# Kernel optimization log

Measured on AMD Instinct MI355X. Metric: run time of the kernel, lower is better.

## Reference

```python
import jax, jax.numpy as jnp
import numpy as np

EPS = 1e-5

def layer_norm(x, g, b):
    mu = jnp.mean(x, axis=-1, keepdims=True)
    var = jnp.mean(jnp.square(x - mu), axis=-1, keepdims=True)
    return (x - mu) * jax.lax.rsqrt(var + EPS) * g + b

def setup_inputs() -> dict:
    key = jax.random.key(0)
    ks = jax.random.split(key, 12)
    I, H, N = 512, 512, 65536
    s = 0.02
    return {
        "x": jax.random.normal(ks[0], (I,), dtype=jnp.float32),
        "hiddens": jax.random.normal(ks[1], (N, H), dtype=jnp.float32),
        "Wz": jax.random.normal(ks[2], (H, I + H), dtype=jnp.float32) * s,
        "Wri": jax.random.normal(ks[3], (H, I), dtype=jnp.float32) * s,
        "Wrh": jax.random.normal(ks[4], (H, H), dtype=jnp.float32) * s,
        "Wu": jax.random.normal(ks[5], (H, I + H), dtype=jnp.float32) * s,
        "gz": jnp.ones((H,), jnp.float32), "bz": jnp.zeros((H,), jnp.float32),
        "gr": jnp.ones((H,), jnp.float32), "br": jnp.zeros((H,), jnp.float32),
        "gu": jnp.ones((H,), jnp.float32), "bu": jnp.zeros((H,), jnp.float32),
    }

def reference(x, hiddens, Wz, Wri, Wrh, Wu, gz, bz, gr, br, gu, bu):
    # hiddens: [N, H] stacked child hidden states; x: [I]
    hidden_sum = hiddens.sum(0)  # [H]
    # r gate: per-child linear + LayerNorm + sigmoid -> [N, H]
    r_pre = x @ Wri.T + hiddens @ Wrh.T  # broadcast input term over children
    r = jax.nn.sigmoid(layer_norm(r_pre, gr, br))
    # z gate over (input, sum of child hiddens)
    z = jax.nn.sigmoid(layer_norm(jnp.concatenate([x, hidden_sum]) @ Wz.T, gz, bz))
    # candidate with reset-gated child sum
    u = jnp.tanh(layer_norm(jnp.concatenate([x, (r * hiddens).sum(0)]) @ Wu.T, gu, bu))
    h = z * hidden_sum + (1.0 - z) * u
    return h
```

## Files before the change

### kernel.cpp

```cpp
#include <hip/hip_runtime.h>

#define HDIM 512
#define BM 128

typedef __attribute__((ext_vector_type(8))) short bf16x8;
typedef __attribute__((ext_vector_type(4))) float f32x4;

__device__ __forceinline__ unsigned short f2bf(float f){
  union { float f; unsigned int u; } c; c.f = f;
  unsigned int u = c.u;
  unsigned int r = u + 0x7fffu + ((u >> 16) & 1u);
  return (unsigned short)(r >> 16);
}
__device__ __forceinline__ float bf2f(unsigned short b){
  union { unsigned int u; float f; } c; c.u = ((unsigned int)b) << 16;
  return c.f;
}
__device__ __forceinline__ unsigned int pack_trunc(float a, float b){
  return __builtin_amdgcn_perm(__float_as_uint(b), __float_as_uint(a), 0x07060302u);
}

__global__ __launch_bounds__(256) void prep_k(const float* __restrict__ Wrh,
    unsigned short* __restrict__ wpack, const float* __restrict__ Wri,
    const float* __restrict__ x, float* __restrict__ xwri)
{
  int b = blockIdx.x;
  if (b < 128){
    int t    = b * 256 + threadIdx.x;
    int lane = t & 63;
    int g    = t >> 6;
    int ni   = g & 3;
    int kkk  = (g >> 2) & 15;
    int wc   = g >> 6;
    int row  = wc * 64 + ni * 16 + (lane & 15);
    int k0   = kkk * 32 + (lane >> 4) * 8;
    const float* src = Wrh + (size_t)row * HDIM + k0;
    float4 f0 = *(const float4*)(src);
    float4 f1 = *(const float4*)(src + 4);
    bf16x8 v;
    v[0]=(short)f2bf(f0.x); v[1]=(short)f2bf(f0.y); v[2]=(short)f2bf(f0.z); v[3]=(short)f2bf(f0.w);
    v[4]=(short)f2bf(f1.x); v[5]=(short)f2bf(f1.y); v[6]=(short)f2bf(f1.z); v[7]=(short)f2bf(f1.w);
    *(bf16x8*)(wpack + (size_t)t * 8) = v;
  } else {
    int lane = threadIdx.x & 63, wid = threadIdx.x >> 6;
    int row = (b - 128) * 4 + wid;
    const float* Wr = Wri + (size_t)row * HDIM;
    float a = 0.f;
    #pragma unroll
    for (int k = 0; k < HDIM / 64; k++) a += x[k*64 + lane] * Wr[k*64 + lane];
    #pragma unroll
    for (int m = 1; m < 64; m <<= 1) a += __shfl_xor(a, m, 64);
    if (lane == 0) xwri[row] = a;
  }
}

__global__ __launch_bounds__(1024, 4) void fused_r(
    const float* __restrict__ hiddens,
    const unsigned short* __restrict__ wpack,
    const float* __restrict__ xWri,
    const float* __restrict__ gr, const float* __restrict__ br,
    float* __restrict__ psum_rh, float* __restrict__ psum_h)
{
  __shared__ short As[BM * HDIM];
  __shared__ float redS[8 * 128];
  __shared__ float redQ[8 * 128];
  __shared__ float mu_s[128], rs_s[128];

  const int tid    = threadIdx.x;
  const int lane   = tid & 63;
  const int wid    = tid >> 6;
  const int rowgrp = wid >> 3;
  const int colgrp = wid & 7;
  const int llo    = lane & 15;
  const int lhi    = lane >> 4;
  const int wcol   = colgrp * 64;
  const int rbase  = rowgrp * 64;
  const int r0     = blockIdx.x * BM;

  const int arow = tid >> 3;
  const int ac8  = (tid & 7) * 8;
  const float* aslice = hiddens + (size_t)(r0 + arow) * HDIM + (tid & 7) * 4;
  char* asb = (char*)As + arow * 1024;
  const int sw = (arow & 7) << 4;

  f32x4 acc[4][4];
  #pragma unroll
  for (int i = 0; i < 4; i++)
    #pragma unroll
    for (int j = 0; j < 4; j++)
      #pragma unroll
      for (int k = 0; k < 4; k++) acc[i][j][k] = 0.f;

  float4 pref0 = *(const float4*)(aslice);
  float4 pref1 = *(const float4*)(aslice + 32);
  const bf16x8* wp = (const bf16x8*)wpack + ((size_t)colgrp * 16 * 4) * 64 + lane;
  bf16x8 bfr[4];
  #pragma unroll
  for (int ni = 0; ni < 4; ni++) bfr[ni] = wp[ni * 64];
  {
    uint2 w; w.x = pack_trunc(pref0.x, pref0.y); w.y = pack_trunc(pref0.z, pref0.w);
    *(uint2*)(asb + (ac8 ^ sw)) = w;
  }
  asm volatile("s_waitcnt lgkmcnt(0)" ::: "memory");
  __builtin_amdgcn_s_barrier();

  #pragma unroll 2
  for (int kb = 0; kb < 16; kb++){
    bf16x8 af[4];
    #pragma unroll
    for (int mi = 0; mi < 4; mi++){
      int row = rbase + mi * 16 + llo;
      af[mi] = *(const bf16x8*)((char*)As + row * 1024
                 + ((kb * 64 + lhi * 16) ^ ((row & 7) << 4)));
    }
    if ((kb & 1) == 0){ if (kb + 2 < 16) pref0 = *(const float4*)(aslice + (kb + 2) * 32); }
    else              { if (kb + 2 < 16) pref1 = *(const float4*)(aslice + (kb + 2) * 32); }
    #pragma unroll
    for (int mi = 0; mi < 4; mi++)
      #pragma unroll
      for (int ni = 0; ni < 4; ni++)
        acc[mi][ni] = __builtin_amdgcn_mfma_f32_16x16x32_bf16(af[mi], bfr[ni], acc[mi][ni], 0, 0, 0);
    if (kb + 1 < 16){
      const bf16x8* wpn = wp + (kb + 1) * 4 * 64;
      #pragma unroll
      for (int ni = 0; ni < 4; ni++) bfr[ni] = wpn[ni * 64];
    }
    if (kb + 1 < 16){
      float4 p = ((kb + 1) & 1) ? pref1 : pref0;
      uint2 w; w.x = pack_trunc(p.x, p.y); w.y = pack_trunc(p.z, p.w);
      *(uint2*)(asb + (((kb + 1) * 64 + ac8) ^ sw)) = w;
    }
    asm volatile("s_waitcnt lgkmcnt(0)" ::: "memory");
    __builtin_amdgcn_s_barrier();
  }

  float xw[4], g4[4], b4[4];
  #pragma unroll
  for (int ni = 0; ni < 4; ni++){
    int c = wcol + ni * 16 + llo;
    xw[ni] = xWri[c];
    g4[ni] = gr[c];
    b4[ni] = br[c];
  }
  #pragma unroll
  for (int mi = 0; mi < 4; mi++){
    #pragma unroll
    for (int rr = 0; rr < 4; rr++){
      float sv = 0.f, qv = 0.f;
      #pragma unroll
      for (int ni = 0; ni < 4; ni++){
        float v = acc[mi][ni][rr] + xw[ni];
        acc[mi][ni][rr] = v;
        sv += v; qv += v * v;
      }
      #pragma unroll
      for (int m = 1; m < 16; m <<= 1){
        sv += __shfl_xor(sv, m, 64);
        qv += __shfl_xor(qv, m, 64);
      }
      if (llo == 0){
        int row = rbase + mi * 16 + lhi * 4 + rr;
        redS[colgrp * 128 + row] = sv;
        redQ[colgrp * 128 + row] = qv;
      }
    }
  }
  __syncthreads();
  if (tid < 128){
    float S = 0.f, Q = 0.f;
    #pragma unroll
    for (int w = 0; w < 8; w++){ S += redS[w * 128 + tid]; Q += redQ[w * 128 + tid]; }
    float mu  = S * (1.f / 512.f);
    float var = Q * (1.f / 512.f) - mu * mu;
    mu_s[tid] = mu;
    rs_s[tid] = rsqrtf(var + 1e-5f);
  }
  __syncthreads();

  float prh[4] = {0.f, 0.f, 0.f, 0.f};
  float ph [4] = {0.f, 0.f, 0.f, 0.f};
  #pragma unroll
  for (int mi = 0; mi < 4; mi++){
    #pragma unroll
    for (int rr = 0; rr < 4; rr++){
      int row = rbase + mi * 16 + lhi * 4 + rr;
      float mu = mu_s[row], rs = rs_s[row];
      int sw2 = (row & 7) << 4;
      #pragma unroll
      for (int ni = 0; ni < 4; ni++){
        float v = (acc[mi][ni][rr] - mu) * rs * g4[ni] + b4[ni];
        float r = __builtin_amdgcn_rcpf(1.f + __expf(-v));
        int col = wcol + ni * 16 + llo;
        float h = bf2f(*(const unsigned short*)((char*)As + row * 1024 + ((col * 2) ^ sw2)));
        prh[ni] += r * h;
        ph [ni] += h;
      }
    }
  }
  #pragma unroll
  for (int ni = 0; ni < 4; ni++){
    prh[ni] += __shfl_xor(prh[ni], 16, 64);
    prh[ni] += __shfl_xor(prh[ni], 32, 64);
    ph [ni] += __shfl_xor(ph [ni], 16, 64);
    ph [ni] += __shfl_xor(ph [ni], 32, 64);
  }
  float* ppRH = redS;
  float* ppH  = redQ;
  if (lhi == 0){
    #pragma unroll
    for (int ni = 0; ni < 4; ni++){
      int col = wcol + ni * 16 + llo;
      ppRH[rowgrp * 512 + col] = prh[ni];
      ppH [rowgrp * 512 + col] = ph[ni];
    }
  }
  __syncthreads();
  if (tid < 512){
    psum_rh[(size_t)blockIdx.x * HDIM + tid] = ppRH[tid] + ppRH[512 + tid];
    psum_h [(size_t)blockIdx.x * HDIM + tid] = ppH[tid]  + ppH[512 + tid];
  }
}

__global__ __launch_bounds__(256) void reduce_psums(
    const float* __restrict__ psum_rh, const float* __restrict__ psum_h,
    const float* __restrict__ x, float* __restrict__ catz, float* __restrict__ catu,
    int nblk)
{
  __shared__ float L[8][32];
  int b = blockIdx.x, t = threadIdx.x;
  if (b < 32){
    const float* P = (b < 16) ? psum_rh : psum_h;
    int c0 = (b & 15) * 32;
    int wj = t >> 5, ci = t & 31;
    float a = 0.f;
    for (int s = wj; s < nblk; s += 8) a += P[(size_t)s * 512 + c0 + ci];
    L[wj][ci] = a;
    __syncthreads();
    if (t < 32){
      float r = 0.f;
      #pragma unroll
      for (int w = 0; w < 8; w++) r += L[w][t];
      if (b < 16) catu[512 + c0 + t] = r;
      else        catz[512 + c0 + t] = r;
    }
  } else {
    int i = ((b - 32) & 1) * 256 + t;
    if (b < 34) catz[i] = x[i];
    else        catu[i] = x[i];
  }
}

__global__ __launch_bounds__(256) void matvec_zu(
    const float* __restrict__ Wz, const float* __restrict__ Wu,
    const float* __restrict__ catz, const float* __restrict__ catu,
    float* __restrict__ zpre, float* __restrict__ upre)
{
  int b = blockIdx.x, lane = threadIdx.x & 63, wid = threadIdx.x >> 6;
  int row = (b & 127) * 4 + wid;
  const float* W = (b < 128) ? Wz : Wu;
  const float* v = (b < 128) ? catz : catu;
  float*       o = (b < 128) ? zpre : upre;
  const float* Wr = W + (size_t)row * 1024;
  float a = 0.f;
  #pragma unroll
  for (int k = 0; k < 1024 / 64; k++) a += v[k*64 + lane] * Wr[k*64 + lane];
  #pragma unroll
  for (int m = 1; m < 64; m <<= 1) a += __shfl_xor(a, m, 64);
  if (lane == 0) o[row] = a;
}

__global__ __launch_bounds__(512) void finalize_k(
    const float* __restrict__ zpre, const float* __restrict__ upre,
    const float* __restrict__ gz, const float* __restrict__ bz,
    const float* __restrict__ gu, const float* __restrict__ bu,
    const float* __restrict__ catz, float* __restrict__ out)
{
  __shared__ float R[8][4];
  int t = threadIdx.x, lane = t & 63, wid = t >> 6;
  float zp = zpre[t], up = upre[t];
  float zs = zp, zq = zp * zp, us = up, uq = up * up;
  #pragma unroll
  for (int m = 1; m < 64; m <<= 1){
    zs += __shfl_xor(zs, m, 64); zq += __shfl_xor(zq, m, 64);
    us += __shfl_xor(us, m, 64); uq += __shfl_xor(uq, m, 64);
  }
  if (lane == 0){ R[wid][0] = zs; R[wid][1] = zq; R[wid][2] = us; R[wid][3] = uq; }
  __syncthreads();
  float ZS = 0.f, ZQ = 0.f, US = 0.f, UQ = 0.f;
  #pragma unroll
  for (int w = 0; w < 8; w++){ ZS += R[w][0]; ZQ += R[w][1]; US += R[w][2]; UQ += R[w][3]; }
  float zmu = ZS / 512.f, zrs = rsqrtf(ZQ / 512.f - zmu * zmu + 1e-5f);
  float umu = US / 512.f, urs = rsqrtf(UQ / 512.f - umu * umu + 1e-5f);
  float z = 1.f / (1.f + expf(-((zp - zmu) * zrs * gz[t] + bz[t])));
  float u = tanhf((up - umu) * urs * gu[t] + bu[t]);
  float hs = catz[512 + t];
  out[t] = z * hs + (1.f - z) * u;
}

extern "C" void kernel_launch(void* const* d_in, const int* in_sizes, int n_in,
                              void* d_out, int out_size, void* d_ws, size_t ws_size,
                              hipStream_t stream)
{
  const float* x   = (const float*)d_in[0];
  const float* hid = (const float*)d_in[1];
  const float* Wz  = (const float*)d_in[2];
  const float* Wri = (const float*)d_in[3];
  const float* Wrh = (const float*)d_in[4];
  const float* Wu  = (const float*)d_in[5];
  const float* gz  = (const float*)d_in[6];
  const float* bz  = (const float*)d_in[7];
  const float* gr  = (const float*)d_in[8];
  const float* br  = (const float*)d_in[9];
  const float* gu  = (const float*)d_in[10];
  const float* bu  = (const float*)d_in[11];
  (void)n_in; (void)out_size; (void)ws_size;

  const int M    = in_sizes[1] / HDIM;
  const int nblk = M / BM;

  char* ws = (char*)d_ws;
  unsigned short* wpack = (unsigned short*)ws;
  float* xwri    = (float*)(ws + 524288);
  float* psum_rh = (float*)(ws + 526336);
  float* psum_h  = (float*)(ws + 526336 + (size_t)nblk * 2048);
  char*  p2      = ws + 526336 + (size_t)nblk * 4096;
  float* catz    = (float*)p2;
  float* catu    = (float*)(p2 + 4096);
  float* zpre    = (float*)(p2 + 8192);
  float* upre    = (float*)(p2 + 10240);
  float* out     = (float*)d_out;

  hipLaunchKernelGGL(prep_k,       dim3(256),  dim3(256),  0, stream, Wrh, wpack, Wri, x, xwri);
  hipLaunchKernelGGL(fused_r,      dim3(nblk), dim3(1024), 0, stream, hid, wpack, xwri, gr, br, psum_rh, psum_h);
  hipLaunchKernelGGL(reduce_psums, dim3(36),   dim3(256),  0, stream, psum_rh, psum_h, x, catz, catu, nblk);
  hipLaunchKernelGGL(matvec_zu,    dim3(256),  dim3(256),  0, stream, Wz, Wu, catz, catu, zpre, upre);
  hipLaunchKernelGGL(finalize_k,   dim3(1),    dim3(512),  0, stream, zpre, upre, gz, bz, gu, bu, catz, out);
}
```

Before: 94.50 us.

## Re-tile shared A buffer into 64-column panels with 16-byte staging writes

Changes the shared-memory layout of the bf16 hidden tile from 1024-byte rows to eight 64-column panels of 128-byte rows, with the XOR swizzle applied inside each panel. Each thread now stages 8 floats per step as a single 16-byte LDS store. The K loop processes two 32-wide k-steps per barrier, so there are 8 barriers instead of 16. The prefetch depth and per-thread global load pattern change accordingly, and the epilogue reads hidden values through the new panel addressing. The goal is fewer barriers, wider LDS writes and simpler read addressing, at the cost of each barrier now covering a larger staged panel.

Result: slower. 133.5 us (+41.3%).

```diff
diff --git a/kernel.cpp b/kernel.cpp
--- a/kernel.cpp
+++ b/kernel.cpp
@@ -77,11 +77,16 @@
   const int rbase  = rowgrp * 64;
   const int r0     = blockIdx.x * BM;
 
-  const int arow = tid >> 3;
-  const int ac8  = (tid & 7) * 8;
-  const float* aslice = hiddens + (size_t)(r0 + arow) * HDIM + (tid & 7) * 4;
-  char* asb = (char*)As + arow * 1024;
-  const int sw = (arow & 7) << 4;
+  const int srow = tid >> 3;
+  const int scs  = tid & 7;
+  const float* aglob = hiddens + (size_t)(r0 + srow) * HDIM + scs * 8;
+  char* const wbase = (char*)As + srow * 128 + ((scs * 16) ^ ((srow & 7) << 4));
+
+  const int swl = (llo & 7) << 4;
+  const char* rdbase[4];
+  #pragma unroll
+  for (int mi = 0; mi < 4; mi++)
+    rdbase[mi] = (char*)As + (rbase + mi * 16 + llo) * 128 + ((lhi * 16) ^ swl);
 
   f32x4 acc[4][4];
   #pragma unroll
@@ -91,44 +96,64 @@
       #pragma unroll
       for (int k = 0; k < 4; k++) acc[i][j][k] = 0.f;
 
-  float4 pref0 = *(const float4*)(aslice);
-  float4 pref1 = *(const float4*)(aslice + 32);
   const bf16x8* wp = (const bf16x8*)wpack + ((size_t)colgrp * 16 * 4) * 64 + lane;
   bf16x8 bfr[4];
   #pragma unroll
   for (int ni = 0; ni < 4; ni++) bfr[ni] = wp[ni * 64];
   {
-    uint2 w; w.x = pack_trunc(pref0.x, pref0.y); w.y = pack_trunc(pref0.z, pref0.w);
-    *(uint2*)(asb + (ac8 ^ sw)) = w;
-  }
+    float4 f0 = *(const float4*)(aglob);
+    float4 f1 = *(const float4*)(aglob + 4);
+    uint4 w;
+    w.x = pack_trunc(f0.x, f0.y); w.y = pack_trunc(f0.z, f0.w);
+    w.z = pack_trunc(f1.x, f1.y); w.w = pack_trunc(f1.z, f1.w);
+    *(uint4*)(wbase) = w;
+  }
+  float4 prefA0 = *(const float4*)(aglob + 64);
+  float4 prefA1 = *(const float4*)(aglob + 68);
   asm volatile("s_waitcnt lgkmcnt(0)" ::: "memory");
   __builtin_amdgcn_s_barrier();
 
   #pragma unroll 2
-  for (int kb = 0; kb < 16; kb++){
-    bf16x8 af[4];
-    #pragma unroll
-    for (int mi = 0; mi < 4; mi++){
-      int row = rbase + mi * 16 + llo;
-      af[mi] = *(const bf16x8*)((char*)As + row * 1024
-                 + ((kb * 64 + lhi * 16) ^ ((row & 7) << 4)));
-    }
-    if ((kb & 1) == 0){ if (kb + 2 < 16) pref0 = *(const float4*)(aslice + (kb + 2) * 32); }
-    else              { if (kb + 2 < 16) pref1 = *(const float4*)(aslice + (kb + 2) * 32); }
+  for (int p = 0; p < 8; p++){
+    const char* const pbase = (const char*)0 + p * 16384;
+    bf16x8 af0[4];
     #pragma unroll
     for (int mi = 0; mi < 4; mi++)
+      af0[mi] = *(const bf16x8*)(rdbase[mi] + (size_t)(pbase - (const char*)0));
+    if (p < 7){
+      uint4 w;
+      w.x = pack_trunc(prefA0.x, prefA0.y); w.y = pack_trunc(prefA0.z, prefA0.w);
+      w.z = pack_trunc(prefA1.x, prefA1.y); w.w = pack_trunc(prefA1.z, prefA1.w);
+      *(uint4*)(wbase + (p + 1) * 16384) = w;
+    }
+    if (p < 6){
+      prefA0 = *(const float4*)(aglob + (p + 2) * 64);
+      prefA1 = *(const float4*)(aglob + (p + 2) * 64 + 4);
+    }
+    #pragma unroll
+    for (int mi = 0; mi < 4; mi++)
       #pragma unroll
       for (int ni = 0; ni < 4; ni++)
-        acc[mi][ni] = __builtin_amdgcn_mfma_f32_16x16x32_bf16(af[mi], bfr[ni], acc[mi][ni], 0, 0, 0);
-    if (kb + 1 < 16){
-      const bf16x8* wpn = wp + (kb + 1) * 4 * 64;
+        acc[mi][ni] = __builtin_amdgcn_mfma_f32_16x16x32_bf16(af0[mi], bfr[ni], acc[mi][ni], 0, 0, 0);
+    {
+      const bf16x8* wpn = wp + (2 * p + 1) * 256;
       #pragma unroll
       for (int ni = 0; ni < 4; ni++) bfr[ni] = wpn[ni * 64];
     }
-    if (kb + 1 < 16){
-      float4 p = ((kb + 1) & 1) ? pref1 : pref0;
-      uint2 w; w.x = pack_trunc(p.x, p.y); w.y = pack_trunc(p.z, p.w);
-      *(uint2*)(asb + (((kb + 1) * 64 + ac8) ^ sw)) = w;
+    bf16x8 af1[4];
+    #pragma unroll
+    for (int mi = 0; mi < 4; mi++)
+      af1[mi] = *(const bf16x8*)((const char*)As +
+                  (((rdbase[mi] - (const char*)As) + p * 16384) ^ 64));
+    #pragma unroll
+    for (int mi = 0; mi < 4; mi++)
+      #pragma unroll
+      for (int ni = 0; ni < 4; ni++)
+        acc[mi][ni] = __builtin_amdgcn_mfma_f32_16x16x32_bf16(af1[mi], bfr[ni], acc[mi][ni], 0, 0, 0);
+    if (p < 7){
+      const bf16x8* wpn = wp + (2 * p + 2) * 256;
+      #pragma unroll
+      for (int ni = 0; ni < 4; ni++) bfr[ni] = wpn[ni * 64];
     }
     asm volatile("s_waitcnt lgkmcnt(0)" ::: "memory");
     __builtin_amdgcn_s_barrier();
@@ -190,8 +215,9 @@
       for (int ni = 0; ni < 4; ni++){
         float v = (acc[mi][ni][rr] - mu) * rs * g4[ni] + b4[ni];
         float r = __builtin_amdgcn_rcpf(1.f + __expf(-v));
-        int col = wcol + ni * 16 + llo;
-        float h = bf2f(*(const unsigned short*)((char*)As + row * 1024 + ((col * 2) ^ sw2)));
+        int cb = (ni * 16 + llo) * 2;
+        float h = bf2f(*(const unsigned short*)((char*)As + colgrp * 16384
+                     + row * 128 + (cb ^ sw2)));
         prh[ni] += r * h;
         ph [ni] += h;
       }
```
